# Optimization experiments

Hardware: AMD Instinct MI355X
Metric: run time of the kernel (lower is better)

## Reference

```python
import jax, jax.numpy as jnp
import numpy as np

B, N, DIM = 4, 8192, 1024
HEADS, DIM_HEAD = 16, 64


def setup_inputs() -> dict:
    key = jax.random.key(0)
    ks = jax.random.split(key, 6)
    s = 1.0 / np.sqrt(DIM_HEAD)
    so = 1.0 / np.sqrt(HEADS * DIM_HEAD)
    return {
        "x": jax.random.normal(ks[0], (B, N, DIM), dtype=jnp.float32),
        "Wq": jax.random.uniform(ks[1], (DIM_HEAD, DIM_HEAD), jnp.float32, -s, s),
        "Wk": jax.random.uniform(ks[2], (DIM_HEAD, DIM_HEAD), jnp.float32, -s, s),
        "Wv": jax.random.uniform(ks[3], (DIM_HEAD, DIM_HEAD), jnp.float32, -s, s),
        "Wo": jax.random.uniform(ks[4], (DIM, HEADS * DIM_HEAD), jnp.float32, -so, so),
        "bo": jax.random.uniform(ks[5], (DIM,), jnp.float32, -so, so),
    }


def reference(x, Wq, Wk, Wv, Wo, bo):
    Bs, Ns, Cs = x.shape
    # [B, H, N, Dh]
    xh = x.reshape(Bs, Ns, HEADS, DIM_HEAD).transpose(0, 2, 1, 3)
    # torch Linear: y = x @ W.T
    q = jnp.einsum('bhnd,ed->bhne', xh, Wq)
    k = jnp.einsum('bhnd,ed->bhne', xh, Wk)
    v = jnp.einsum('bhnd,ed->bhne', xh, Wv)
    # k^T v: [B, H, Dh, Dh], normalized by N (dropout is identity, p=0)
    dots = jnp.einsum('bhnd,bhne->bhde', k, v) / float(Ns)
    res = jnp.einsum('bhnd,bhde->bhne', q, dots)
    # b h n d -> b n (h d)
    res = res.transpose(0, 2, 1, 3).reshape(Bs, Ns, HEADS * DIM_HEAD)
    return res @ Wo.T + bo
```

## Files before the change

kernel.cpp:

```cpp
#include <hip/hip_runtime.h>

#define DIMC 1024
#define NSEQ 8192
#define DH 64

typedef __attribute__((ext_vector_type(8))) short short8;
typedef __attribute__((ext_vector_type(4))) float f32x4;

__device__ __forceinline__ short f2bf(float f) {
  union { float f; unsigned u; } v; v.f = f;
  unsigned r = v.u + 0x7FFFu + ((v.u >> 16) & 1u);
  return (short)(r >> 16);
}

__device__ __forceinline__ unsigned pack_bf2(float a, float b) {
  union { float f; unsigned u; } va, vb;
  va.f = a; vb.f = b;
  unsigned ua = va.u + 0x8000u;
  unsigned ub = vb.u + 0x8000u;
  return (ua >> 16) | (ub & 0xFFFF0000u);
}

__device__ __forceinline__ unsigned bfbits(float f) {
  union { float f; unsigned u; } v; v.f = f;
  return (v.u + 0x8000u) >> 16;
}
__device__ __forceinline__ float bf2f(unsigned hb) {
  union { unsigned u; float f; } v; v.u = hb << 16;
  return v.f;
}

__device__ __forceinline__ void gload_lds16(const void* g, void* l) {
  __builtin_amdgcn_global_load_lds(
      (const __attribute__((address_space(1))) void*)g,
      (__attribute__((address_space(3))) void*)l, 16, 0, 0);
}

__global__ __launch_bounds__(256) void gram2_kernel(const float* __restrict__ x,
                                                    float* __restrict__ Gpart,
                                                    short* __restrict__ xbf) {
  int chunk = blockIdx.x, bh = blockIdx.y;
  int b = bh >> 4, h = bh & 15;
  int t = threadIdx.x;
  int w = t >> 6, l = t & 63;
  int quad = l >> 4, ln = l & 15;

  __shared__ __align__(16) short XT[4][2][64 * 32];
  __shared__ __align__(16) float Pred[3][4096];
  short* XH = &XT[w][0][0];
  short* XL = &XT[w][1][0];

  size_t rowbase = (size_t)b * NSEQ + (size_t)chunk * 1024 + w * 256;
  const float* xb = x + rowbase * DIMC + h * DH;
  short* xo = xbf + rowbase * DIMC + h * DH;

  f32x4 acc[4][4];
#pragma unroll
  for (int i = 0; i < 4; i++)
#pragma unroll
    for (int j = 0; j < 4; j++) acc[i][j] = (f32x4){0.f, 0.f, 0.f, 0.f};

  int woff[4][4];
#pragma unroll
  for (int q = 0; q < 4; q++) {
    int kk = 8 * q + 2 * quad;
    int kp = kk ^ ((ln & 3) << 3);
#pragma unroll
    for (int i = 0; i < 4; i++) {
      int d = ln * 4 + i;
      woff[q][i] = d * 32 + kp;
    }
  }
  int roff[4];
  {
    int k0 = (quad * 8) ^ ((ln >> 2) << 3);
#pragma unroll
    for (int i = 0; i < 4; i++) roff[i] = (i * 16 + ln) * 32 + k0;
  }

  float4 cur[4][2];
#pragma unroll
  for (int q = 0; q < 4; q++)
#pragma unroll
    for (int r = 0; r < 2; r++)
      cur[q][r] = *(const float4*)(xb + (size_t)(8 * q + 2 * quad + r) * DIMC + ln * 4);

  for (int ks = 0; ks < 8; ks++) {
    float4 nxt[4][2];
    if (ks < 7) {
      int nb = (ks + 1) * 32;
#pragma unroll
      for (int q = 0; q < 4; q++)
#pragma unroll
        for (int r = 0; r < 2; r++)
          nxt[q][r] = *(const float4*)(xb + (size_t)(nb + 8 * q + 2 * quad + r) * DIMC + ln * 4);
    }
#pragma unroll
    for (int q = 0; q < 4; q++) {
      unsigned h0[4], h1[4], l0[4], l1[4];
#pragma unroll
      for (int i = 0; i < 4; i++) {
        float a = cur[q][0][i], bb = cur[q][1][i];
        h0[i] = bfbits(a); l0[i] = bfbits(a - bf2f(h0[i]));
        h1[i] = bfbits(bb); l1[i] = bfbits(bb - bf2f(h1[i]));
      }
      int grow = ks * 32 + 8 * q + 2 * quad;
      uint2 p0 = {h0[0] | (h0[1] << 16), h0[2] | (h0[3] << 16)};
      uint2 p1 = {h1[0] | (h1[1] << 16), h1[2] | (h1[3] << 16)};
      *(uint2*)(xo + (size_t)grow * DIMC + ln * 4) = p0;
      *(uint2*)(xo + (size_t)(grow + 1) * DIMC + ln * 4) = p1;
#pragma unroll
      for (int i = 0; i < 4; i++) {
        *(unsigned*)&XH[woff[q][i]] = h0[i] | (h1[i] << 16);
        *(unsigned*)&XL[woff[q][i]] = l0[i] | (l1[i] << 16);
      }
    }
    short8 hf[4], lf[4];
#pragma unroll
    for (int i = 0; i < 4; i++) {
      hf[i] = *(const short8*)&XH[roff[i]];
      lf[i] = *(const short8*)&XL[roff[i]];
    }
#pragma unroll
    for (int i = 0; i < 4; i++)
#pragma unroll
      for (int j = 0; j < 4; j++) {
        acc[i][j] = __builtin_amdgcn_mfma_f32_16x16x32_bf16(hf[i], hf[j], acc[i][j], 0, 0, 0);
        acc[i][j] = __builtin_amdgcn_mfma_f32_16x16x32_bf16(hf[i], lf[j], acc[i][j], 0, 0, 0);
        acc[i][j] = __builtin_amdgcn_mfma_f32_16x16x32_bf16(lf[i], hf[j], acc[i][j], 0, 0, 0);
      }
#pragma unroll
    for (int q = 0; q < 4; q++)
#pragma unroll
      for (int r = 0; r < 2; r++) cur[q][r] = nxt[q][r];
  }

  if (w > 0) {
    float* pd = &Pred[w - 1][0];
#pragma unroll
    for (int i = 0; i < 4; i++)
#pragma unroll
      for (int j = 0; j < 4; j++)
#pragma unroll
        for (int r = 0; r < 4; r++) {
          int d = i * 16 + quad * 4 + r, e = j * 16 + ln;
          pd[d * 64 + e] = acc[i][j][r];
        }
  }
  __syncthreads();
  if (w == 0) {
    float* gp = Gpart + (size_t)chunk * (64 * 4096) + (size_t)bh * 4096;
#pragma unroll
    for (int i = 0; i < 4; i++)
#pragma unroll
      for (int j = 0; j < 4; j++)
#pragma unroll
        for (int r = 0; r < 4; r++) {
          int d = i * 16 + quad * 4 + r, e = j * 16 + ln;
          int idx = d * 64 + e;
          gp[idx] = acc[i][j][r] + Pred[0][idx] + Pred[1][idx] + Pred[2][idx];
        }
  }
}

__global__ __launch_bounds__(64) void gram_kernel(const float* __restrict__ x,
                                                  float* __restrict__ Gpart,
                                                  short* __restrict__ xbf) {
  int chunk = blockIdx.x, bh = blockIdx.y;
  int b = bh >> 4, h = bh & 15;
  int t = threadIdx.x;
  __shared__ __align__(16) float rows[16 * 64];
  const float* xb = x + ((size_t)b * NSEQ) * DIMC + h * DH;
  short* xo = xbf ? xbf + ((size_t)b * NSEQ) * DIMC + h * DH : (short*)0;
  int d0 = (t >> 3) * 8, e0 = (t & 7) * 8;
  float acc[8][8] = {};
  float4 v[4];
#pragma unroll
  for (int i = 0; i < 4; i++) {
    int f4 = i * 64 + t;
    v[i] = *(const float4*)(xb + (size_t)(chunk * 256 + (f4 >> 4)) * DIMC + (f4 & 15) * 4);
  }
  for (int it = 0; it < 16; it++) {
    __syncthreads();
#pragma unroll
    for (int i = 0; i < 4; i++) ((float4*)rows)[i * 64 + t] = v[i];
    __syncthreads();
    if (xo) {
#pragma unroll
      for (int i = 0; i < 4; i++) {
        int f4 = i * 64 + t;
        int row = chunk * 256 + it * 16 + (f4 >> 4), col = (f4 & 15) * 4;
        uint2 pw = {pack_bf2(v[i].x, v[i].y), pack_bf2(v[i].z, v[i].w)};
        *(uint2*)(xo + (size_t)row * DIMC + col) = pw;
      }
    }
    if (it < 15) {
      int nbase = chunk * 256 + (it + 1) * 16;
#pragma unroll
      for (int i = 0; i < 4; i++) {
        int f4 = i * 64 + t;
        v[i] = *(const float4*)(xb + (size_t)(nbase + (f4 >> 4)) * DIMC + (f4 & 15) * 4);
      }
    }
#pragma unroll
    for (int r = 0; r < 16; r++) {
      float xd[8], xe[8];
      *(float4*)&xd[0] = *(const float4*)&rows[r * 64 + d0];
      *(float4*)&xd[4] = *(const float4*)&rows[r * 64 + d0 + 4];
      *(float4*)&xe[0] = *(const float4*)&rows[r * 64 + e0];
      *(float4*)&xe[4] = *(const float4*)&rows[r * 64 + e0 + 4];
#pragma unroll
      for (int i = 0; i < 8; i++)
#pragma unroll
        for (int j = 0; j < 8; j++) acc[i][j] = fmaf(xd[i], xe[j], acc[i][j]);
    }
  }
  float* gp = Gpart + (size_t)chunk * (64 * 4096) + (size_t)bh * 4096;
#pragma unroll
  for (int i = 0; i < 8; i++)
#pragma unroll
    for (int j = 0; j < 8; j++) gp[(d0 + i) * 64 + e0 + j] = acc[i][j];
}

__global__ void reduce_g(const float* __restrict__ Gpart, float* __restrict__ G,
                         int np) {
  int i = blockIdx.x * 256 + threadIdx.x;
  float s = 0.f;
  for (int p = 0; p < np; p++) s += Gpart[(size_t)p * (64 * 4096) + i];
  G[i] = s;
}

__global__ __launch_bounds__(256) void combine_kernel(
    const float* __restrict__ G, const float* __restrict__ Wq,
    const float* __restrict__ Wk, const float* __restrict__ Wv,
    const float* __restrict__ Wo, short* __restrict__ WbigT) {
  int bh = blockIdx.x, qt = blockIdx.y;
  int b = bh >> 4, h = bh & 15;
  int t = threadIdx.x;
  __shared__ __align__(16) float sG[4096];
  __shared__ __align__(16) float sW[4096];
  __shared__ __align__(16) float sA[4096];
  __shared__ __align__(16) float sM[4096];

  for (int i = t; i < 4096; i += 256) sG[i] = G[(size_t)bh * 4096 + i];
  for (int i = t; i < 4096; i += 256) sW[i] = Wk[i];
  __syncthreads();

  int d0 = (t >> 4) * 4, e0 = (t & 15) * 4;
  {
    float a[4][4] = {};
    for (int fg = 0; fg < 16; fg++) {
      float wk[4][4], g4[4][4];
#pragma unroll
      for (int i = 0; i < 4; i++) *(float4*)wk[i] = *(const float4*)&sW[(d0 + i) * 64 + fg * 4];
#pragma unroll
      for (int ff = 0; ff < 4; ff++) *(float4*)g4[ff] = *(const float4*)&sG[(fg * 4 + ff) * 64 + e0];
#pragma unroll
      for (int i = 0; i < 4; i++)
#pragma unroll
        for (int ff = 0; ff < 4; ff++)
#pragma unroll
          for (int j = 0; j < 4; j++) a[i][j] = fmaf(wk[i][ff], g4[ff][j], a[i][j]);
    }
#pragma unroll
    for (int i = 0; i < 4; i++)
#pragma unroll
      for (int j = 0; j < 4; j++) sA[(d0 + i) * 64 + e0 + j] = a[i][j];
  }
  __syncthreads();
  for (int i = t; i < 4096; i += 256) sW[i] = Wv[i];
  __syncthreads();
  {
    float a[4][4] = {};
    for (int fgi = 0; fgi < 16; fgi++) {
      int fg = (fgi + (t & 15)) & 15;
      float t1[4][4], wv[4][4];
#pragma unroll
      for (int i = 0; i < 4; i++) *(float4*)t1[i] = *(const float4*)&sA[(d0 + i) * 64 + fg * 4];
#pragma unroll
      for (int j = 0; j < 4; j++) *(float4*)wv[j] = *(const float4*)&sW[(e0 + j) * 64 + fg * 4];
#pragma unroll
      for (int i = 0; i < 4; i++)
#pragma unroll
        for (int j = 0; j < 4; j++)
#pragma unroll
          for (int ff = 0; ff < 4; ff++) a[i][j] = fmaf(t1[i][ff], wv[j][ff], a[i][j]);
    }
    __syncthreads();
#pragma unroll
    for (int i = 0; i < 4; i++)
#pragma unroll
      for (int j = 0; j < 4; j++) sG[(d0 + i) * 64 + e0 + j] = a[i][j];
  }
  __syncthreads();
  for (int i = t; i < 4096; i += 256) sW[i] = Wq[i];
  __syncthreads();
  {
    float a[4][4] = {};
    for (int f = 0; f < 64; f++) {
      float wq[4], t2[4];
      *(float4*)wq = *(const float4*)&sW[f * 64 + d0];
      *(float4*)t2 = *(const float4*)&sG[f * 64 + e0];
#pragma unroll
      for (int i = 0; i < 4; i++)
#pragma unroll
        for (int j = 0; j < 4; j++) a[i][j] = fmaf(wq[i], t2[j], a[i][j]);
    }
#pragma unroll
    for (int i = 0; i < 4; i++)
#pragma unroll
      for (int j = 0; j < 4; j++) sM[(d0 + i) * 64 + e0 + j] = a[i][j] * (1.0f / 8192.0f);
  }
  __syncthreads();
  int dd0 = (t & 15) * 4, cl0 = (t >> 4) * 4;
  for (int cc = qt * 2; cc < qt * 2 + 2; cc++) {
    int c0 = cc * 64;
    for (int i = t; i < 4096; i += 256)
      sW[i] = Wo[(size_t)(c0 + (i >> 6)) * DIMC + h * DH + (i & 63)];
    __syncthreads();
    float a[4][4] = {};
    for (int egi = 0; egi < 16; egi++) {
      int eg = (egi + (t & 15)) & 15;
      float m4[4][4], wo4[4][4];
#pragma unroll
      for (int i = 0; i < 4; i++) *(float4*)m4[i] = *(const float4*)&sM[(dd0 + i) * 64 + eg * 4];
#pragma unroll
      for (int j = 0; j < 4; j++) *(float4*)wo4[j] = *(const float4*)&sW[(cl0 + j) * 64 + eg * 4];
#pragma unroll
      for (int i = 0; i < 4; i++)
#pragma unroll
        for (int j = 0; j < 4; j++)
#pragma unroll
          for (int ff = 0; ff < 4; ff++) a[i][j] = fmaf(m4[i][ff], wo4[j][ff], a[i][j]);
    }
#pragma unroll
    for (int j = 0; j < 4; j++) {
      uint2 pw = {pack_bf2(a[0][j], a[1][j]), pack_bf2(a[2][j], a[3][j])};
      *(uint2*)&WbigT[((size_t)b << 20) + (size_t)(c0 + cl0 + j) * DIMC + h * DH + dd0] = pw;
    }
    __syncthreads();
  }
}

__global__ __launch_bounds__(256, 3) void gemm_small(
    const float* __restrict__ x, const short* __restrict__ WbigT,
    const float* __restrict__ bo, float* __restrict__ out) {
  int bid = blockIdx.x;
  int xcd = bid & 7, r = bid >> 3;
  int g = r >> 5, q = r & 31;
  int m_blk = g * 32 + xcd * 4 + (q >> 3);
  int n_blk = q & 7;
  int b = m_blk >> 6;
  int row0 = m_blk * 128;
  int c0 = n_blk * 128;

  __shared__ __align__(16) short As[128 * 32];
  __shared__ __align__(16) short Bs[128 * 32];

  int t = threadIdx.x;
  int lane = t & 63, wave = t >> 6;
  int wm = wave >> 1, wn = wave & 1;
  int quad = lane >> 4, ln = lane & 15;

  f32x4 acc[4][4];
#pragma unroll
  for (int i = 0; i < 4; i++)
#pragma unroll
    for (int j = 0; j < 4; j++) acc[i][j] = (f32x4){0.f, 0.f, 0.f, 0.f};

  const short* Bbase = WbigT + ((size_t)b << 20);

  int e_base[2], crow_[2], lc_[2];
#pragma unroll
  for (int L = 0; L < 2; L++) {
    int e = (wave * 2 + L) * 512 + lane * 8;
    e_base[L] = e;
    int crow = e >> 5;
    crow_[L] = crow;
    lc_[L] = ((e >> 3) & 3) ^ ((crow >> 1) & 3);
  }

  for (int kt = 0; kt < 32; kt++) {
    int k0 = kt * 32;
    __syncthreads();
#pragma unroll
    for (int L = 0; L < 2; L++)
      gload_lds16(Bbase + (size_t)(c0 + crow_[L]) * DIMC + k0 + lc_[L] * 8, &Bs[e_base[L]]);
#pragma unroll
    for (int qq = 0; qq < 2; qq++) {
      int elem = qq * 2048 + wave * 512 + lane * 8;
      int m = elem >> 5, kk = elem & 31;
      const float* gp = x + (size_t)(row0 + m) * DIMC + k0 + kk;
      float4 v0 = *(const float4*)gp;
      float4 v1 = *(const float4*)(gp + 4);
      unsigned w0 = pack_bf2(v0.x, v0.y), w1 = pack_bf2(v0.z, v0.w);
      unsigned w2 = pack_bf2(v1.x, v1.y), w3 = pack_bf2(v1.z, v1.w);
      unsigned tmp[4] = {w0, w1, w2, w3};
      int pe = ((elem >> 3) & 3) ^ ((m >> 1) & 3);
      *(short8*)&As[m * 32 + pe * 8] = *(short8*)tmp;
    }
    __syncthreads();
    short8 afrag[4], bfrag[4];
#pragma unroll
    for (int i = 0; i < 4; i++) {
      int ar = wm * 64 + i * 16 + ln;
      afrag[i] = *(const short8*)&As[ar * 32 + (quad ^ ((ar >> 1) & 3)) * 8];
      int br = wn * 64 + i * 16 + ln;
      bfrag[i] = *(const short8*)&Bs[br * 32 + (quad ^ ((br >> 1) & 3)) * 8];
    }
#pragma unroll
    for (int i = 0; i < 4; i++)
#pragma unroll
      for (int j = 0; j < 4; j++)
        acc[i][j] = __builtin_amdgcn_mfma_f32_16x16x32_bf16(afrag[i], bfrag[j], acc[i][j], 0, 0, 0);
  }

  float bov[4];
#pragma unroll
  for (int j = 0; j < 4; j++) bov[j] = bo[c0 + wn * 64 + j * 16 + ln];
#pragma unroll
  for (int i = 0; i < 4; i++)
#pragma unroll
    for (int j = 0; j < 4; j++) {
      int col = c0 + wn * 64 + j * 16 + ln;
#pragma unroll
      for (int rr = 0; rr < 4; rr++) {
        int row = row0 + wm * 64 + i * 16 + quad * 4 + rr;
        out[(size_t)row * DIMC + col] = acc[i][j][rr] + bov[j];
      }
    }
}

__global__ __launch_bounds__(256, 3) void gemm_big(
    const short* __restrict__ xbf, const short* __restrict__ WbigT,
    const float* __restrict__ bo, float* __restrict__ out) {
  int bid = blockIdx.x;
  int xcd = bid & 7, r = bid >> 3;
  int g = r >> 5, q = r & 31;
  int m_blk = g * 32 + xcd * 4 + (q >> 3);
  int n_blk = q & 7;
  int b = m_blk >> 6;
  int row0 = m_blk * 128;
  int c0 = n_blk * 128;

  __shared__ __align__(16) short As[128 * 32];
  __shared__ __align__(16) short Bs[128 * 32];

  int t = threadIdx.x;
  int lane = t & 63, wave = t >> 6;
  int wm = wave >> 1, wn = wave & 1;
  int quad = lane >> 4, ln = lane & 15;

  f32x4 acc[4][4];
#pragma unroll
  for (int i = 0; i < 4; i++)
#pragma unroll
    for (int j = 0; j < 4; j++) acc[i][j] = (f32x4){0.f, 0.f, 0.f, 0.f};

  const short* Bbase = WbigT + ((size_t)b << 20);

  int e_base[2];
  const short* Asrc[2];
  const short* Bsrc[2];
#pragma unroll
  for (int L = 0; L < 2; L++) {
    int e = (wave * 2 + L) * 512 + lane * 8;
    e_base[L] = e;
    int row = e >> 5;
    int lc = ((e >> 3) & 3) ^ ((row >> 1) & 3);
    Asrc[L] = xbf + (size_t)(row0 + row) * DIMC + lc * 8;
    Bsrc[L] = Bbase + (size_t)(c0 + row) * DIMC + lc * 8;
  }

  for (int kt = 0; kt < 32; kt++) {
    int k0 = kt * 32;
    __syncthreads();
#pragma unroll
    for (int L = 0; L < 2; L++) gload_lds16(Asrc[L] + k0, &As[e_base[L]]);
#pragma unroll
    for (int L = 0; L < 2; L++) gload_lds16(Bsrc[L] + k0, &Bs[e_base[L]]);
    __syncthreads();
    short8 afrag[4], bfrag[4];
#pragma unroll
    for (int i = 0; i < 4; i++) {
      int ar = wm * 64 + i * 16 + ln;
      afrag[i] = *(const short8*)&As[ar * 32 + (quad ^ ((ar >> 1) & 3)) * 8];
      int br = wn * 64 + i * 16 + ln;
      bfrag[i] = *(const short8*)&Bs[br * 32 + (quad ^ ((br >> 1) & 3)) * 8];
    }
#pragma unroll
    for (int i = 0; i < 4; i++)
#pragma unroll
      for (int j = 0; j < 4; j++)
        acc[i][j] = __builtin_amdgcn_mfma_f32_16x16x32_bf16(afrag[i], bfrag[j], acc[i][j], 0, 0, 0);
  }

  float bov[4];
#pragma unroll
  for (int j = 0; j < 4; j++) bov[j] = bo[c0 + wn * 64 + j * 16 + ln];
#pragma unroll
  for (int i = 0; i < 4; i++)
#pragma unroll
    for (int j = 0; j < 4; j++) {
      int col = c0 + wn * 64 + j * 16 + ln;
#pragma unroll
      for (int rr = 0; rr < 4; rr++) {
        int row = row0 + wm * 64 + i * 16 + quad * 4 + rr;
        out[(size_t)row * DIMC + col] = acc[i][j][rr] + bov[j];
      }
    }
}

extern "C" void kernel_launch(void* const* d_in, const int* in_sizes, int n_in,
                              void* d_out, int out_size, void* d_ws, size_t ws_size,
                              hipStream_t stream) {
  const float* x  = (const float*)d_in[0];
  const float* Wq = (const float*)d_in[1];
  const float* Wk = (const float*)d_in[2];
  const float* Wv = (const float*)d_in[3];
  const float* Wo = (const float*)d_in[4];
  const float* bo = (const float*)d_in[5];
  float* out = (float*)d_out;
  (void)in_sizes; (void)n_in; (void)out_size;

  if (ws_size >= ((size_t)81 << 20)) {
    short* xbf   = (short*)d_ws;
    float* Gpart = (float*)((char*)d_ws + ((size_t)64 << 20));
    float* G     = (float*)((char*)d_ws + ((size_t)72 << 20));
    short* WbigT = (short*)((char*)d_ws + ((size_t)73 << 20));
    gram2_kernel<<<dim3(8, 64), 256, 0, stream>>>(x, Gpart, xbf);
    reduce_g<<<1024, 256, 0, stream>>>(Gpart, G, 8);
    combine_kernel<<<dim3(64, 8), 256, 0, stream>>>(G, Wq, Wk, Wv, Wo, WbigT);
    gemm_big<<<2048, 256, 0, stream>>>(xbf, WbigT, bo, out);
  } else {
    float* Gpart = (float*)d_ws;
    float* G     = (float*)((char*)d_ws + ((size_t)32 << 20));
    short* WbigT = (short*)((char*)d_ws + ((size_t)33 << 20));
    gram_kernel<<<dim3(32, 64), 64, 0, stream>>>(x, Gpart, (short*)0);
    reduce_g<<<1024, 256, 0, stream>>>(Gpart, G, 32);
    combine_kernel<<<dim3(64, 8), 256, 0, stream>>>(G, Wq, Wk, Wv, Wo, WbigT);
    gemm_small<<<2048, 256, 0, stream>>>(x, WbigT, bo, out);
  }
}
```

Measured before the change: 363.1 us.

## Fold Gram reduction into per-head M computation and split Wbig build

The separate Gpart reduction kernel is removed, and the partial-Gram sum is folded into a new per-(batch,head) kernel. That kernel computes the small 64x64 product Wq^T·(Wk·G·Wv^T)/N once and writes M to workspace. A second kernel then forms the bf16 WbigT tiles from M and Wo. Before, the combine kernel likely recomputed the M chain in each of its 8 qt blocks, so this avoids that redundant work and one launch. The cost is an extra launch boundary and an M round-trip through global memory, and compute_m runs on only 64 blocks.

```diff
diff --git a/kernel.cpp b/kernel.cpp
--- a/kernel.cpp
+++ b/kernel.cpp
@@ -230,6 +230,136 @@
   G[i] = s;
 }
 
+__global__ __launch_bounds__(256) void compute_m_kernel(
+    const float* __restrict__ Gpart, const float* __restrict__ Wq,
+    const float* __restrict__ Wk, const float* __restrict__ Wv,
+    float* __restrict__ M) {
+  int bh = blockIdx.x;
+  int t = threadIdx.x;
+  __shared__ __align__(16) float sG[4096];
+  __shared__ __align__(16) float sW[4096];
+  __shared__ __align__(16) float sA[4096];
+
+  for (int i = t; i < 4096; i += 256) {
+    float s = 0.f;
+#pragma unroll
+    for (int p = 0; p < 8; p++)
+      s += Gpart[(size_t)p * (64 * 4096) + (size_t)bh * 4096 + i];
+    sG[i] = s;
+  }
+  for (int i = t; i < 4096; i += 256) sW[i] = Wk[i];
+  __syncthreads();
+
+  int d0 = (t >> 4) * 4, e0 = (t & 15) * 4;
+  {
+    float a[4][4] = {};
+    for (int fg = 0; fg < 16; fg++) {
+      float wk[4][4], g4[4][4];
+#pragma unroll
+      for (int i = 0; i < 4; i++) *(float4*)wk[i] = *(const float4*)&sW[(d0 + i) * 64 + fg * 4];
+#pragma unroll
+      for (int ff = 0; ff < 4; ff++) *(float4*)g4[ff] = *(const float4*)&sG[(fg * 4 + ff) * 64 + e0];
+#pragma unroll
+      for (int i = 0; i < 4; i++)
+#pragma unroll
+        for (int ff = 0; ff < 4; ff++)
+#pragma unroll
+          for (int j = 0; j < 4; j++) a[i][j] = fmaf(wk[i][ff], g4[ff][j], a[i][j]);
+    }
+#pragma unroll
+    for (int i = 0; i < 4; i++)
+#pragma unroll
+      for (int j = 0; j < 4; j++) sA[(d0 + i) * 64 + e0 + j] = a[i][j];
+  }
+  __syncthreads();
+  for (int i = t; i < 4096; i += 256) sW[i] = Wv[i];
+  __syncthreads();
+  {
+    float a[4][4] = {};
+    for (int fgi = 0; fgi < 16; fgi++) {
+      int fg = (fgi + (t & 15)) & 15;
+      float t1[4][4], wv[4][4];
+#pragma unroll
+      for (int i = 0; i < 4; i++) *(float4*)t1[i] = *(const float4*)&sA[(d0 + i) * 64 + fg * 4];
+#pragma unroll
+      for (int j = 0; j < 4; j++) *(float4*)wv[j] = *(const float4*)&sW[(e0 + j) * 64 + fg * 4];
+#pragma unroll
+      for (int i = 0; i < 4; i++)
+#pragma unroll
+        for (int j = 0; j < 4; j++)
+#pragma unroll
+          for (int ff = 0; ff < 4; ff++) a[i][j] = fmaf(t1[i][ff], wv[j][ff], a[i][j]);
+    }
+    __syncthreads();
+#pragma unroll
+    for (int i = 0; i < 4; i++)
+#pragma unroll
+      for (int j = 0; j < 4; j++) sG[(d0 + i) * 64 + e0 + j] = a[i][j];
+  }
+  __syncthreads();
+  for (int i = t; i < 4096; i += 256) sW[i] = Wq[i];
+  __syncthreads();
+  {
+    float a[4][4] = {};
+    for (int f = 0; f < 64; f++) {
+      float wq[4], t2[4];
+      *(float4*)wq = *(const float4*)&sW[f * 64 + d0];
+      *(float4*)t2 = *(const float4*)&sG[f * 64 + e0];
+#pragma unroll
+      for (int i = 0; i < 4; i++)
+#pragma unroll
+        for (int j = 0; j < 4; j++) a[i][j] = fmaf(wq[i], t2[j], a[i][j]);
+    }
+    float* mo = M + (size_t)bh * 4096;
+#pragma unroll
+    for (int i = 0; i < 4; i++)
+#pragma unroll
+      for (int j = 0; j < 4; j++)
+        mo[(d0 + i) * 64 + e0 + j] = a[i][j] * (1.0f / 8192.0f);
+  }
+}
+
+__global__ __launch_bounds__(256) void wbig_kernel(
+    const float* __restrict__ M, const float* __restrict__ Wo,
+    short* __restrict__ WbigT) {
+  int bh = blockIdx.x, qt = blockIdx.y;
+  int b = bh >> 4, h = bh & 15;
+  int t = threadIdx.x;
+  __shared__ __align__(16) float sM[4096];
+  __shared__ __align__(16) float sW[4096];
+
+  for (int i = t; i < 4096; i += 256) sM[i] = M[(size_t)bh * 4096 + i];
+
+  int dd0 = (t & 15) * 4, cl0 = (t >> 4) * 4;
+  for (int cc = qt * 2; cc < qt * 2 + 2; cc++) {
+    int c0 = cc * 64;
+    for (int i = t; i < 4096; i += 256)
+      sW[i] = Wo[(size_t)(c0 + (i >> 6)) * DIMC + h * DH + (i & 63)];
+    __syncthreads();
+    float a[4][4] = {};
+    for (int egi = 0; egi < 16; egi++) {
+      int eg = (egi + (t & 15)) & 15;
+      float m4[4][4], wo4[4][4];
+#pragma unroll
+      for (int i = 0; i < 4; i++) *(float4*)m4[i] = *(const float4*)&sM[(dd0 + i) * 64 + eg * 4];
+#pragma unroll
+      for (int j = 0; j < 4; j++) *(float4*)wo4[j] = *(const float4*)&sW[(cl0 + j) * 64 + eg * 4];
+#pragma unroll
+      for (int i = 0; i < 4; i++)
+#pragma unroll
+        for (int j = 0; j < 4; j++)
+#pragma unroll
+          for (int ff = 0; ff < 4; ff++) a[i][j] = fmaf(m4[i][ff], wo4[j][ff], a[i][j]);
+    }
+#pragma unroll
+    for (int j = 0; j < 4; j++) {
+      uint2 pw = {pack_bf2(a[0][j], a[1][j]), pack_bf2(a[2][j], a[3][j])};
+      *(uint2*)&WbigT[((size_t)b << 20) + (size_t)(c0 + cl0 + j) * DIMC + h * DH + dd0] = pw;
+    }
+    __syncthreads();
+  }
+}
+
 __global__ __launch_bounds__(256) void combine_kernel(
     const float* __restrict__ G, const float* __restrict__ Wq,
     const float* __restrict__ Wk, const float* __restrict__ Wv,
@@ -526,11 +656,11 @@
   if (ws_size >= ((size_t)81 << 20)) {
     short* xbf   = (short*)d_ws;
     float* Gpart = (float*)((char*)d_ws + ((size_t)64 << 20));
-    float* G     = (float*)((char*)d_ws + ((size_t)72 << 20));
+    float* M     = (float*)((char*)d_ws + ((size_t)72 << 20));
     short* WbigT = (short*)((char*)d_ws + ((size_t)73 << 20));
     gram2_kernel<<<dim3(8, 64), 256, 0, stream>>>(x, Gpart, xbf);
-    reduce_g<<<1024, 256, 0, stream>>>(Gpart, G, 8);
-    combine_kernel<<<dim3(64, 8), 256, 0, stream>>>(G, Wq, Wk, Wv, Wo, WbigT);
+    compute_m_kernel<<<64, 256, 0, stream>>>(Gpart, Wq, Wk, Wv, M);
+    wbig_kernel<<<dim3(64, 8), 256, 0, stream>>>(M, Wo, WbigT);
     gemm_big<<<2048, 256, 0, stream>>>(xbf, WbigT, bo, out);
   } else {
     float* Gpart = (float*)d_ws;
```

New measurement: 367.8 us. No clear change (+1.3%).
